# Kernel tuning notes

Measured on AMD Instinct MI355X. Metric: run time of the kernel, lower is better.

## Reference

```python
import jax, jax.numpy as jnp
import numpy as np

T = 4096   # reference sequence length (concatenated virtual samples)
L = 4096   # modality sequence length
D_Q = 64   # reference feature dim
D_QK = 128 # projected query/key dim (before add_one -> 129)
D_V = 128  # value dim
N_IDS = 8  # number of virtual samples encoded in idx


def setup_inputs() -> dict:
    key = jax.random.key(0)
    ks = jax.random.split(key, 20)
    inp = {}
    inp['ref_data'] = jax.random.normal(ks[0], (1, 1, T, D_Q), jnp.float32)
    inp['ref_time'] = jnp.sort(jax.random.uniform(ks[1], (1, T), jnp.float32), axis=-1)
    inp['ref_idx'] = jnp.sort(jax.random.randint(ks[2], (T,), 0, N_IDS))
    inp['m1_data'] = jax.random.normal(ks[3], (1, 1, L, 130), jnp.float32)
    inp['m1_time'] = jnp.sort(jax.random.uniform(ks[4], (1, L), jnp.float32), axis=-1)
    inp['m1_idx'] = jnp.sort(jax.random.randint(ks[5], (L,), 0, N_IDS))
    inp['m2_data'] = jax.random.normal(ks[6], (1, 1, L, 66), jnp.float32)
    inp['m2_time'] = jnp.sort(jax.random.uniform(ks[7], (1, L), jnp.float32), axis=-1)
    inp['m2_idx'] = jnp.sort(jax.random.randint(ks[8], (L,), 0, N_IDS))
    s = 0.05
    inp['Wq'] = jax.random.normal(ks[9], (D_Q, D_QK), jnp.float32) * s
    inp['bq'] = jnp.zeros((D_QK,), jnp.float32)
    inp['Wk1'] = jax.random.normal(ks[10], (1, D_QK), jnp.float32) * s
    inp['bk1'] = jnp.zeros((D_QK,), jnp.float32)
    inp['Wv1'] = jax.random.normal(ks[11], (128, D_V), jnp.float32) * s
    inp['bv1'] = jnp.zeros((D_V,), jnp.float32)
    inp['Wk2'] = jax.random.normal(ks[12], (1, D_QK), jnp.float32) * s
    inp['bk2'] = jnp.zeros((D_QK,), jnp.float32)
    inp['Wv2'] = jax.random.normal(ks[13], (64, D_V), jnp.float32) * s
    inp['bv2'] = jnp.zeros((D_V,), jnp.float32)
    inp['log_tau1'] = jnp.zeros((), jnp.float32)  # log(init_tau=1)
    inp['log_tau2'] = jnp.zeros((), jnp.float32)
    return inp


def _add_one_q(x):  # add_one(x, dim=1): append ones on last axis
    return jnp.concatenate([x, jnp.ones(x.shape[:-1] + (1,), x.dtype)], axis=-1)


def _feat_k(x):  # add_one(x, dim=0): [ones, -x]
    return jnp.concatenate([jnp.ones(x.shape[:-1] + (1,), x.dtype), -x], axis=-1)


def _uni_attn(Q, mdata, q_t, kv_t, q_idx, kv_idx, Wk, bk, Wv, bv, log_tau):
    # qk_type='time': keys from last feature (timestamp), values from data[..., :-2]
    K = _feat_k(mdata[..., -1:] @ Wk + bk)          # (1,1,L,d_qk+1)
    V = mdata[..., :-2] @ Wv + bv                   # (1,1,L,d_v)
    tau = jnp.exp(log_tau)
    # gaussian weight: -(Q.K)^2 / tau
    A = -jnp.square(jnp.einsum('nhtc,nhlc->nhtl', Q, K)) / tau  # (1,1,T,L)
    causal = (q_t[:, :, None] >= kv_t[:, None, :]).astype(Q.dtype)[:, None]  # (1,1,T,L)
    neg_inf = jnp.array(-jnp.inf, Q.dtype)
    bm = jnp.where(q_idx[None, :, None] == kv_idx[None, None, :], jnp.zeros((), Q.dtype), neg_inf)  # (1,T,L)
    fully_masked = jnp.all(jnp.isneginf(bm), axis=-1, keepdims=True)
    safe = jnp.where(fully_masked, jnp.zeros((), Q.dtype), bm)[:, None]  # (1,1,T,L)
    A = jax.nn.softmax(A * causal + safe, axis=-1) * causal
    return jnp.einsum('nhtl,nhlc->nhtc', A, V)      # (1,1,T,d_v)


def reference(ref_data, ref_time, m1_data, m1_time, m2_data, m2_time,
              Wq, bq, Wk1, bk1, Wv1, bv1, Wk2, bk2, Wv2, bv2,
              log_tau1, log_tau2, ref_idx, m1_idx, m2_idx):
    Q = _add_one_q(ref_data @ Wq + bq)  # (1,1,T,d_qk+1)
    y1 = _uni_attn(Q, m1_data, ref_time, m1_time, ref_idx, m1_idx, Wk1, bk1, Wv1, bv1, log_tau1)
    y2 = _uni_attn(Q, m2_data, ref_time, m2_time, ref_idx, m2_idx, Wk2, bk2, Wv2, bv2, log_tau2)
    return jnp.concatenate([y1, y2], axis=-1)  # (1,1,T,2*d_v)
```

## Files before the change

kernel.cpp:

```cpp
#include <hip/hip_runtime.h>
#include <hip/hip_bf16.h>

#define TQ 4096
#define LK 4096
#define QT 16
#define NSPLIT 4
#define CHJ 16
#define PB 32
#define PQ (TQ / PB)
#define VPB 512

template<bool BF> __device__ __forceinline__ float ld(const void* p, int i);
template<> __device__ __forceinline__ float ld<true>(const void* p, int i) {
    return __bfloat162float(((const __hip_bfloat16*)p)[i]);
}
template<> __device__ __forceinline__ float ld<false>(const void* p, int i) {
    return ((const float*)p)[i];
}
template<bool BF> __device__ __forceinline__ float2 ld2(const void* p, int i);
template<> __device__ __forceinline__ float2 ld2<false>(const void* p, int i) {
    return *(const float2*)((const float*)p + i);
}
template<> __device__ __forceinline__ float2 ld2<true>(const void* p, int i) {
    float2 r; r.x = ld<true>(p, i); r.y = ld<true>(p, i + 1); return r;
}
template<bool BF> __device__ __forceinline__ float4 ld4(const void* p, int i);
template<> __device__ __forceinline__ float4 ld4<false>(const void* p, int i) {
    return *(const float4*)((const float*)p + i);
}
template<> __device__ __forceinline__ float4 ld4<true>(const void* p, int i) {
    float4 r; r.x = ld<true>(p, i); r.y = ld<true>(p, i + 1);
    r.z = ld<true>(p, i + 2); r.w = ld<true>(p, i + 3); return r;
}
template<bool BF> __device__ __forceinline__ void st4(void* p, int i, float4 v);
template<> __device__ __forceinline__ void st4<true>(void* p, int i, float4 v) {
    __hip_bfloat16* o = (__hip_bfloat16*)p + i;
    o[0] = __float2bfloat16(v.x); o[1] = __float2bfloat16(v.y);
    o[2] = __float2bfloat16(v.z); o[3] = __float2bfloat16(v.w);
}
template<> __device__ __forceinline__ void st4<false>(void* p, int i, float4 v) {
    *(float4*)((float*)p + i) = v;
}

__device__ __forceinline__ bool sniff_bf16(const void* ref_time) {
    const int lane = threadIdx.x & 63;
    bool ok = true;
    if (lane < 32) {
        float v = __bfloat162float(((const __hip_bfloat16*)ref_time)[2 * lane]);
        ok = (v >= 0.0f) && (v <= 1.0f);
    }
    return __ballot(ok) == ~0ULL;
}

__device__ int lb_int(const int* arr, int n, int key) {
    int lo = 0, hi = n;
    while (lo < hi) { int mid = (lo + hi) >> 1; if (arr[mid] < key) lo = mid + 1; else hi = mid; }
    return lo;
}
__device__ int ub_int(const int* arr, int n, int key) {
    int lo = 0, hi = n;
    while (lo < hi) { int mid = (lo + hi) >> 1; if (arr[mid] <= key) lo = mid + 1; else hi = mid; }
    return lo;
}

template<bool BF>
__device__ void prep_part(
    const void* ref_data, const void* ref_time, const int* ref_idx,
    const void* m1_time, const int* m1_idx, const void* m2_time, const int* m2_idx,
    const void* Wq, const void* bq,
    const void* Wk1, const void* bk1, const void* Wk2, const void* bk2,
    float* alpha1, float* beta1, float* alpha2, float* beta2,
    int* c1, int* s1, int* e1, int* c2, int* s2, int* e2)
{
    __shared__ float ut[64][4];
    __shared__ float cst[4];
    __shared__ int tabs[4][8];

    const int tid = threadIdx.x;
    const int i = tid >> 2, r = tid & 3;

    {
        const void* w = (r == 0) ? Wk1 : (r == 1) ? bk1 : (r == 2) ? Wk2 : bk2;
        const bool isA = (r & 1);
        float acc = isA ? ld<BF>(Wq, i * 128) : 0.0f;
        const float sgn = isA ? -1.0f : 1.0f;
        #pragma unroll 4
        for (int d = 1; d < 128; ++d)
            acc = fmaf(sgn * ld<BF>(Wq, i * 128 + d), ld<BF>(w, d - 1), acc);
        ut[i][r] = acc;
    }
    if (tid < 4) {
        const void* w = (tid == 0) ? Wk1 : (tid == 1) ? bk1 : (tid == 2) ? Wk2 : bk2;
        const bool isA = (tid & 1);
        float c = isA ? ld<BF>(bq, 0) : 0.0f;
        const float sgn = isA ? -1.0f : 1.0f;
        #pragma unroll 4
        for (int d = 1; d < 128; ++d)
            c = fmaf(sgn * ld<BF>(bq, d), ld<BF>(w, d - 1), c);
        c += sgn * ld<BF>(w, 127);
        cst[tid] = c;
    }
    if (tid >= 4 && tid < 36) {
        const int k = tid - 4;
        const int sid = k & 7, rest = k >> 3;
        const int modk = rest & 1, kind = rest >> 1;
        const int* arr = modk ? m2_idx : m1_idx;
        tabs[modk * 2 + kind][sid] = kind ? ub_int(arr, LK, sid) : lb_int(arr, LK, sid);
    }
    __syncthreads();

    const int q = tid & 127;
    const int t = blockIdx.x * PQ + q;
    if (tid < 128) {
        float4 acc = {cst[0], cst[1], cst[2], cst[3]};
        #pragma unroll
        for (int ii = 0; ii < 64; ii += 4) {
            const float4 rv = ld4<BF>(ref_data, t * 64 + ii);
            const float4 u0 = *(const float4*)ut[ii + 0];
            const float4 u1 = *(const float4*)ut[ii + 1];
            const float4 u2 = *(const float4*)ut[ii + 2];
            const float4 u3 = *(const float4*)ut[ii + 3];
            acc.x = fmaf(rv.x, u0.x, fmaf(rv.y, u1.x, fmaf(rv.z, u2.x, fmaf(rv.w, u3.x, acc.x))));
            acc.y = fmaf(rv.x, u0.y, fmaf(rv.y, u1.y, fmaf(rv.z, u2.y, fmaf(rv.w, u3.y, acc.y))));
            acc.z = fmaf(rv.x, u0.z, fmaf(rv.y, u1.z, fmaf(rv.z, u2.z, fmaf(rv.w, u3.z, acc.z))));
            acc.w = fmaf(rv.x, u0.w, fmaf(rv.y, u1.w, fmaf(rv.z, u2.w, fmaf(rv.w, u3.w, acc.w))));
        }
        beta1[t] = acc.x; alpha1[t] = acc.y;
        beta2[t] = acc.z; alpha2[t] = acc.w;
    } else {
        const float qt = ld<BF>(ref_time, t);
        const int g = ref_idx[t];
        int lo1 = 0, hi1 = LK, lo2 = 0, hi2 = LK;
        #pragma unroll
        for (int it = 0; it < 13; ++it) {
            const int mA = min((lo1 + hi1) >> 1, LK - 1);
            const int mB = min((lo2 + hi2) >> 1, LK - 1);
            const float v1 = ld<BF>(m1_time, mA);
            const float v2 = ld<BF>(m2_time, mB);
            if (lo1 < hi1) { if (v1 <= qt) lo1 = mA + 1; else hi1 = mA; }
            if (lo2 < hi2) { if (v2 <= qt) lo2 = mB + 1; else hi2 = mB; }
        }
        c1[t] = lo1; c2[t] = lo2;
        s1[t] = tabs[0][g]; e1[t] = tabs[1][g];
        s2[t] = tabs[2][g]; e2[t] = tabs[3][g];
    }
}

template<bool BF, int K, int DM>
__device__ void vproj_wave(const void* md, const void* Wv, const void* bv,
                           float* V, float* X, int rows0)
{
    const int lane = threadIdx.x & 63;
    const int cT = lane & 31;
    const int rG = lane >> 5;
    const int r0 = rows0 + rG * 2;
    const int c4 = cT * 4;

    const float4 bb = ld4<BF>(bv, c4);
    float4 acc[2] = {bb, bb};

    #pragma unroll 4
    for (int k = 0; k < K; k += 4) {
        const float4 w0 = ld4<BF>(Wv, (k + 0) * 128 + c4);
        const float4 w1 = ld4<BF>(Wv, (k + 1) * 128 + c4);
        const float4 w2 = ld4<BF>(Wv, (k + 2) * 128 + c4);
        const float4 w3 = ld4<BF>(Wv, (k + 3) * 128 + c4);
        float2 alo[2], ahi[2];
        #pragma unroll
        for (int r = 0; r < 2; ++r) {
            alo[r] = ld2<BF>(md, (r0 + r) * DM + k);
            ahi[r] = ld2<BF>(md, (r0 + r) * DM + k + 2);
        }
        #pragma unroll
        for (int r = 0; r < 2; ++r) {
            acc[r].x = fmaf(alo[r].x, w0.x, fmaf(alo[r].y, w1.x, fmaf(ahi[r].x, w2.x, fmaf(ahi[r].y, w3.x, acc[r].x))));
            acc[r].y = fmaf(alo[r].x, w0.y, fmaf(alo[r].y, w1.y, fmaf(ahi[r].x, w2.y, fmaf(ahi[r].y, w3.y, acc[r].y))));
            acc[r].z = fmaf(alo[r].x, w0.z, fmaf(alo[r].y, w1.z, fmaf(ahi[r].x, w2.z, fmaf(ahi[r].y, w3.z, acc[r].z))));
            acc[r].w = fmaf(alo[r].x, w0.w, fmaf(alo[r].y, w1.w, fmaf(ahi[r].x, w2.w, fmaf(ahi[r].y, w3.w, acc[r].w))));
        }
    }
    #pragma unroll
    for (int r = 0; r < 2; ++r)
        *(float4*)&V[(size_t)(r0 + r) * 128 + c4] = acc[r];
    if (rG == 0 && cT < 4)
        X[rows0 + cT] = ld<BF>(md, (rows0 + cT) * DM + DM - 1);
}

template<bool BF>
__device__ void pv_body(
    const void* ref_data, const void* ref_time, const int* ref_idx,
    const void* m1_data, const void* m1_time, const int* m1_idx,
    const void* m2_data, const void* m2_time, const int* m2_idx,
    const void* Wq, const void* bq,
    const void* Wk1, const void* bk1, const void* Wk2, const void* bk2,
    const void* Wv1, const void* bv1, const void* Wv2, const void* bv2,
    float* alpha1, float* beta1, float* alpha2, float* beta2,
    int* c1, int* s1, int* e1, int* c2, int* s2, int* e2,
    float* V1, float* V2, float* X1, float* X2)
{
    if (blockIdx.x < PB) {
        prep_part<BF>(ref_data, ref_time, ref_idx, m1_time, m1_idx, m2_time, m2_idx,
                      Wq, bq, Wk1, bk1, Wk2, bk2,
                      alpha1, beta1, alpha2, beta2, c1, s1, e1, c2, s2, e2);
    } else {
        const int vb = blockIdx.x - PB;
        const int mod = vb >> 8;
        const int wid = threadIdx.x >> 6;
        const int rows0 = (vb & 255) * 16 + wid * 4;
        if (mod == 0) vproj_wave<BF, 128, 130>(m1_data, Wv1, bv1, V1, X1, rows0);
        else          vproj_wave<BF, 64, 66>(m2_data, Wv2, bv2, V2, X2, rows0);
    }
}

__global__ __launch_bounds__(256) void pv_kernel(
    const void* ref_data, const void* ref_time, const int* ref_idx,
    const void* m1_data, const void* m1_time, const int* m1_idx,
    const void* m2_data, const void* m2_time, const int* m2_idx,
    const void* Wq, const void* bq,
    const void* Wk1, const void* bk1, const void* Wk2, const void* bk2,
    const void* Wv1, const void* bv1, const void* Wv2, const void* bv2,
    float* alpha1, float* beta1, float* alpha2, float* beta2,
    int* c1, int* s1, int* e1, int* c2, int* s2, int* e2,
    float* V1, float* V2, float* X1, float* X2)
{
    if (sniff_bf16(ref_time))
        pv_body<true>(ref_data, ref_time, ref_idx, m1_data, m1_time, m1_idx,
                      m2_data, m2_time, m2_idx, Wq, bq, Wk1, bk1, Wk2, bk2,
                      Wv1, bv1, Wv2, bv2, alpha1, beta1, alpha2, beta2,
                      c1, s1, e1, c2, s2, e2, V1, V2, X1, X2);
    else
        pv_body<false>(ref_data, ref_time, ref_idx, m1_data, m1_time, m1_idx,
                       m2_data, m2_time, m2_idx, Wq, bq, Wk1, bk1, Wk2, bk2,
                       Wv1, bv1, Wv2, bv2, alpha1, beta1, alpha2, beta2,
                       c1, s1, e1, c2, s2, e2, V1, V2, X1, X2);
}

__global__ __launch_bounds__(128) void attn_kernel(
    const void* __restrict__ ref_time,
    const float* __restrict__ alpha1, const float* __restrict__ beta1,
    const float* __restrict__ alpha2, const float* __restrict__ beta2,
    const int* __restrict__ c1, const int* __restrict__ s1, const int* __restrict__ e1,
    const int* __restrict__ c2, const int* __restrict__ s2, const int* __restrict__ e2,
    const float* __restrict__ V1, const float* __restrict__ V2,
    const float* __restrict__ X1, const float* __restrict__ X2,
    const void* log_tau1, const void* log_tau2,
    float* __restrict__ Opart, float* __restrict__ Zpart)
{
    __shared__ float sW[2][CHJ * QT];
    __shared__ float sO[QT * 128];
    __shared__ float sZm[QT];

    const int tid = threadIdx.x;
    const int wid = tid >> 6, lane = tid & 63;
    const int t0 = blockIdx.x * QT, zb = blockIdx.y, mod = blockIdx.z;

    const bool bf = sniff_bf16(ref_time);
    const float* alpha = mod ? alpha2 : alpha1;
    const float* beta  = mod ? beta2  : beta1;
    const int* cA = mod ? c2 : c1;
    const int* sA = mod ? s2 : s1;
    const int* eA = mod ? e2 : e1;
    const float* V = mod ? V2 : V1;
    const float* X = mod ? X2 : X1;
    const void* ltp = mod ? log_tau2 : log_tau1;
    const float scale = __expf(-(bf ? ld<true>(ltp, 0) : ld<false>(ltp, 0)));

    const int q = lane & 15;
    const int t = t0 + q;
    int s = sA[t], e = eA[t];
    const int c = cA[t];
    if (s == e) { s = 0; e = LK; }
    const int cm = min(c, e);
    const float al = alpha[t], be = beta[t];

    int es = (cm > s) ? s : 0x7fffffff;
    int ec = (cm > s) ? cm : 0;
    #pragma unroll
    for (int o = 1; o < 64; o <<= 1) {
        es = min(es, __shfl_xor(es, o));
        ec = max(ec, __shfl_xor(ec, o));
    }
    int jlo = es, jhi = ec;
    if (jlo > jhi) { jlo = 0; jhi = 0; }
    const int W = jhi - jlo;
    const int chunk = (W + NSPLIT * 2 - 1) / (NSPLIT * 2);
    const int sub = zb * 2 + wid;
    const int lo = jlo + sub * chunk;
    int hi = min(jhi, lo + chunk); if (hi < lo) hi = lo;

    const int cT = lane & 31, qG = lane >> 5;
    const int jj = lane >> 4;
    float4 acc[8] = {{0,0,0,0},{0,0,0,0},{0,0,0,0},{0,0,0,0},
                     {0,0,0,0},{0,0,0,0},{0,0,0,0},{0,0,0,0}};
    float zacc = 0.0f;
    float* myW = sW[wid];
    const float4* __restrict__ Vg = (const float4*)V;

    for (int base = lo; base < hi; base += CHJ) {
        const int jm = min(CHJ, hi - base);
        __asm__ volatile("s_waitcnt lgkmcnt(0)" ::: "memory");
        #pragma unroll
        for (int p = 0; p < 4; ++p) {
            const int jr = jj * 4 + p;
            const int j = base + jr;
            const bool ok = (jr < jm) && (j >= s) && (j < cm);
            const float x = X[min(j, LK - 1)];
            const float qk = fmaf(-be, x, al);
            const float w = ok ? __expf(-(qk * qk) * scale) : 0.0f;
            myW[jr * QT + q] = w;
            zacc += w;
        }
        __asm__ volatile("s_waitcnt lgkmcnt(0)" ::: "memory");
        #pragma unroll 4
        for (int j = 0; j < jm; ++j) {
            const float4 v = Vg[(base + j) * 32 + cT];
            const float4* wv = (const float4*)&myW[j * QT + qG * 8];
            const float4 wA = wv[0], wB = wv[1];
            acc[0].x = fmaf(wA.x, v.x, acc[0].x); acc[0].y = fmaf(wA.x, v.y, acc[0].y);
            acc[0].z = fmaf(wA.x, v.z, acc[0].z); acc[0].w = fmaf(wA.x, v.w, acc[0].w);
            acc[1].x = fmaf(wA.y, v.x, acc[1].x); acc[1].y = fmaf(wA.y, v.y, acc[1].y);
            acc[1].z = fmaf(wA.y, v.z, acc[1].z); acc[1].w = fmaf(wA.y, v.w, acc[1].w);
            acc[2].x = fmaf(wA.z, v.x, acc[2].x); acc[2].y = fmaf(wA.z, v.y, acc[2].y);
            acc[2].z = fmaf(wA.z, v.z, acc[2].z); acc[2].w = fmaf(wA.z, v.w, acc[2].w);
            acc[3].x = fmaf(wA.w, v.x, acc[3].x); acc[3].y = fmaf(wA.w, v.y, acc[3].y);
            acc[3].z = fmaf(wA.w, v.z, acc[3].z); acc[3].w = fmaf(wA.w, v.w, acc[3].w);
            acc[4].x = fmaf(wB.x, v.x, acc[4].x); acc[4].y = fmaf(wB.x, v.y, acc[4].y);
            acc[4].z = fmaf(wB.x, v.z, acc[4].z); acc[4].w = fmaf(wB.x, v.w, acc[4].w);
            acc[5].x = fmaf(wB.y, v.x, acc[5].x); acc[5].y = fmaf(wB.y, v.y, acc[5].y);
            acc[5].z = fmaf(wB.y, v.z, acc[5].z); acc[5].w = fmaf(wB.y, v.w, acc[5].w);
            acc[6].x = fmaf(wB.z, v.x, acc[6].x); acc[6].y = fmaf(wB.z, v.y, acc[6].y);
            acc[6].z = fmaf(wB.z, v.z, acc[6].z); acc[6].w = fmaf(wB.z, v.w, acc[6].w);
            acc[7].x = fmaf(wB.w, v.x, acc[7].x); acc[7].y = fmaf(wB.w, v.y, acc[7].y);
            acc[7].z = fmaf(wB.w, v.z, acc[7].z); acc[7].w = fmaf(wB.w, v.w, acc[7].w);
        }
    }

    float z = zacc;
    z += __shfl_xor(z, 16);
    z += __shfl_xor(z, 32);

    const int part = zb * 2 + mod;
    if (wid == 0) {
        #pragma unroll
        for (int r = 0; r < 8; ++r)
            *(float4*)&sO[(qG * 8 + r) * 128 + cT * 4] = acc[r];
        if (lane < 16) sZm[lane] = z;
    }
    __syncthreads();
    if (wid == 1) {
        float4* Og = (float4*)Opart;
        #pragma unroll
        for (int r = 0; r < 8; ++r) {
            const float4 o0 = *(const float4*)&sO[(qG * 8 + r) * 128 + cT * 4];
            float4 o = acc[r];
            o.x += o0.x; o.y += o0.y; o.z += o0.z; o.w += o0.w;
            Og[((size_t)(part << 12) + (t0 + qG * 8 + r)) * 32 + cT] = o;
        }
        if (lane < 16) Zpart[(part << 12) + t0 + lane] = z + sZm[lane];
    }
}

__global__ __launch_bounds__(256) void finish_kernel(
    const void* __restrict__ ref_time,
    const int* __restrict__ c1, const int* __restrict__ s1, const int* __restrict__ e1,
    const int* __restrict__ c2, const int* __restrict__ s2, const int* __restrict__ e2,
    const float* __restrict__ Zpart, const float* __restrict__ Opart,
    void* __restrict__ out)
{
    const bool bf = sniff_bf16(ref_time);
    const int idx = blockIdx.x * 256 + threadIdx.x;
    const int t = idx >> 6;
    const int rem = idx & 63;
    const int mod = rem >> 5;
    const int c4 = rem & 31;

    const int* cA = mod ? c2 : c1;
    const int* sA = mod ? s2 : s1;
    const int* eA = mod ? e2 : e1;
    int s = sA[t], e = eA[t];
    const int c = cA[t];
    if (s == e) { s = 0; e = LK; }
    const int nnc = (e > c) ? (e - max(s, c)) : 0;

    float Z = (float)nnc;
    float4 o = {0, 0, 0, 0};
    const float4* Og = (const float4*)Opart;
    #pragma unroll
    for (int zb = 0; zb < NSPLIT; ++zb) {
        const int part = zb * 2 + mod;
        Z += Zpart[(part << 12) + t];
        const float4 p = Og[((size_t)(part << 12) + t) * 32 + c4];
        o.x += p.x; o.y += p.y; o.z += p.z; o.w += p.w;
    }
    const float inv = 1.0f / fmaxf(Z, 1.0e-20f);
    o.x *= inv; o.y *= inv; o.z *= inv; o.w *= inv;
    if (bf) st4<true>(out, t * 256 + mod * 128 + c4 * 4, o);
    else    st4<false>(out, t * 256 + mod * 128 + c4 * 4, o);
}

extern "C" void kernel_launch(void* const* d_in, const int* in_sizes, int n_in,
                              void* d_out, int out_size, void* d_ws, size_t ws_size,
                              hipStream_t stream)
{
    const void* ref_data = d_in[0];
    const void* ref_time = d_in[1];
    const int*  ref_idx  = (const int*)d_in[2];
    const void* m1_data  = d_in[3];
    const void* m1_time  = d_in[4];
    const int*  m1_idx   = (const int*)d_in[5];
    const void* m2_data  = d_in[6];
    const void* m2_time  = d_in[7];
    const int*  m2_idx   = (const int*)d_in[8];
    const void* Wq  = d_in[9];
    const void* bq  = d_in[10];
    const void* Wk1 = d_in[11];
    const void* bk1 = d_in[12];
    const void* Wv1 = d_in[13];
    const void* bv1 = d_in[14];
    const void* Wk2 = d_in[15];
    const void* bk2 = d_in[16];
    const void* Wv2 = d_in[17];
    const void* bv2 = d_in[18];
    const void* log_tau1 = d_in[19];
    const void* log_tau2 = d_in[20];

    float* ws = (float*)d_ws;
    float* alpha1 = ws + 0 * TQ;
    float* beta1  = ws + 1 * TQ;
    float* alpha2 = ws + 2 * TQ;
    float* beta2  = ws + 3 * TQ;
    int*   c1 = (int*)(ws + 4 * TQ);
    int*   c2 = (int*)(ws + 5 * TQ);
    int*   s1 = (int*)(ws + 6 * TQ);
    int*   e1 = (int*)(ws + 7 * TQ);
    int*   s2 = (int*)(ws + 8 * TQ);
    int*   e2 = (int*)(ws + 9 * TQ);
    float* X1 = ws + 10 * TQ;
    float* X2 = ws + 11 * TQ;
    float* V1 = ws + 12 * TQ;
    float* V2 = V1 + (size_t)LK * 128;
    float* Zpart = V2 + (size_t)LK * 128;
    float* Opart = Zpart + 8 * TQ;

    pv_kernel<<<dim3(PB + VPB), dim3(256), 0, stream>>>(
        ref_data, ref_time, ref_idx, m1_data, m1_time, m1_idx,
        m2_data, m2_time, m2_idx, Wq, bq, Wk1, bk1, Wk2, bk2,
        Wv1, bv1, Wv2, bv2, alpha1, beta1, alpha2, beta2,
        c1, s1, e1, c2, s2, e2, V1, V2, X1, X2);

    attn_kernel<<<dim3(TQ / QT, NSPLIT, 2), dim3(128), 0, stream>>>(
        ref_time, alpha1, beta1, alpha2, beta2, c1, s1, e1, c2, s2, e2,
        V1, V2, X1, X2, log_tau1, log_tau2, Opart, Zpart);

    finish_kernel<<<dim3(TQ * 2 * 32 / 256), dim3(256), 0, stream>>>(
        ref_time, c1, s1, e1, c2, s2, e2, Zpart, Opart, (void*)d_out);
}
```

Before: 164.1 us.

## Fuse split-K reduction into attention kernel using 8 waves per block

Replaces the grid-level split over key chunks (4 blocks of 2 waves each, plus a separate finish kernel reading partials from global memory) with a single 512-thread block per query tile and modality. The 8 waves each cover one key sub-range, write their partial outputs and normalizers to shared memory, and then reduce and normalize in-block before writing the final output. This removes one kernel launch and the global round trip of the partial buffers, at the cost of about 70KB of shared memory per block and four times fewer blocks, which may lower occupancy.

```diff
diff --git a/kernel.cpp b/kernel.cpp
--- a/kernel.cpp
+++ b/kernel.cpp
@@ -4,7 +4,7 @@
 #define TQ 4096
 #define LK 4096
 #define QT 16
-#define NSPLIT 4
+#define NW 8
 #define CHJ 16
 #define PB 32
 #define PQ (TQ / PB)
@@ -235,7 +235,7 @@
                        c1, s1, e1, c2, s2, e2, V1, V2, X1, X2);
 }
 
-__global__ __launch_bounds__(128) void attn_kernel(
+__global__ __launch_bounds__(512) void attn_kernel(
     const void* __restrict__ ref_time,
     const float* __restrict__ alpha1, const float* __restrict__ beta1,
     const float* __restrict__ alpha2, const float* __restrict__ beta2,
@@ -243,16 +243,15 @@
     const int* __restrict__ c2, const int* __restrict__ s2, const int* __restrict__ e2,
     const float* __restrict__ V1, const float* __restrict__ V2,
     const float* __restrict__ X1, const float* __restrict__ X2,
-    const void* log_tau1, const void* log_tau2,
-    float* __restrict__ Opart, float* __restrict__ Zpart)
-{
-    __shared__ float sW[2][CHJ * QT];
-    __shared__ float sO[QT * 128];
-    __shared__ float sZm[QT];
+    const void* log_tau1, const void* log_tau2, void* __restrict__ out)
+{
+    __shared__ float sW[NW][CHJ * QT];
+    __shared__ float sO[NW][QT * 128];
+    __shared__ float sZ[NW][QT];
 
     const int tid = threadIdx.x;
     const int wid = tid >> 6, lane = tid & 63;
-    const int t0 = blockIdx.x * QT, zb = blockIdx.y, mod = blockIdx.z;
+    const int t0 = blockIdx.x * QT, mod = blockIdx.y;
 
     const bool bf = sniff_bf16(ref_time);
     const float* alpha = mod ? alpha2 : alpha1;
@@ -283,9 +282,8 @@
     int jlo = es, jhi = ec;
     if (jlo > jhi) { jlo = 0; jhi = 0; }
     const int W = jhi - jlo;
-    const int chunk = (W + NSPLIT * 2 - 1) / (NSPLIT * 2);
-    const int sub = zb * 2 + wid;
-    const int lo = jlo + sub * chunk;
+    const int chunk = (W + NW - 1) / NW;
+    const int lo = jlo + wid * chunk;
     int hi = min(jhi, lo + chunk); if (hi < lo) hi = lo;
 
     const int cT = lane & 31, qG = lane >> 5;
@@ -339,63 +337,31 @@
     z += __shfl_xor(z, 16);
     z += __shfl_xor(z, 32);
 
-    const int part = zb * 2 + mod;
-    if (wid == 0) {
-        #pragma unroll
-        for (int r = 0; r < 8; ++r)
-            *(float4*)&sO[(qG * 8 + r) * 128 + cT * 4] = acc[r];
-        if (lane < 16) sZm[lane] = z;
-    }
+    #pragma unroll
+    for (int r = 0; r < 8; ++r)
+        *(float4*)&sO[wid][(qG * 8 + r) * 128 + cT * 4] = acc[r];
+    if (lane < 16) sZ[wid][lane] = z;
     __syncthreads();
-    if (wid == 1) {
-        float4* Og = (float4*)Opart;
-        #pragma unroll
-        for (int r = 0; r < 8; ++r) {
-            const float4 o0 = *(const float4*)&sO[(qG * 8 + r) * 128 + cT * 4];
-            float4 o = acc[r];
-            o.x += o0.x; o.y += o0.y; o.z += o0.z; o.w += o0.w;
-            Og[((size_t)(part << 12) + (t0 + qG * 8 + r)) * 32 + cT] = o;
-        }
-        if (lane < 16) Zpart[(part << 12) + t0 + lane] = z + sZm[lane];
-    }
-}
-
-__global__ __launch_bounds__(256) void finish_kernel(
-    const void* __restrict__ ref_time,
-    const int* __restrict__ c1, const int* __restrict__ s1, const int* __restrict__ e1,
-    const int* __restrict__ c2, const int* __restrict__ s2, const int* __restrict__ e2,
-    const float* __restrict__ Zpart, const float* __restrict__ Opart,
-    void* __restrict__ out)
-{
-    const bool bf = sniff_bf16(ref_time);
-    const int idx = blockIdx.x * 256 + threadIdx.x;
-    const int t = idx >> 6;
-    const int rem = idx & 63;
-    const int mod = rem >> 5;
-    const int c4 = rem & 31;
-
-    const int* cA = mod ? c2 : c1;
-    const int* sA = mod ? s2 : s1;
-    const int* eA = mod ? e2 : e1;
-    int s = sA[t], e = eA[t];
-    const int c = cA[t];
-    if (s == e) { s = 0; e = LK; }
-    const int nnc = (e > c) ? (e - max(s, c)) : 0;
-
-    float Z = (float)nnc;
+
+    const int mq = tid >> 5, mc = tid & 31;
+    const int mt = t0 + mq;
+    int ms = sA[mt], me = eA[mt];
+    const int mcau = cA[mt];
+    if (ms == me) { ms = 0; me = LK; }
+    const int mnnc = (me > mcau) ? (me - max(ms, mcau)) : 0;
+
+    float Z = (float)mnnc;
     float4 o = {0, 0, 0, 0};
-    const float4* Og = (const float4*)Opart;
     #pragma unroll
-    for (int zb = 0; zb < NSPLIT; ++zb) {
-        const int part = zb * 2 + mod;
-        Z += Zpart[(part << 12) + t];
-        const float4 p = Og[((size_t)(part << 12) + t) * 32 + c4];
+    for (int w = 0; w < NW; ++w) {
+        Z += sZ[w][mq];
+        const float4 p = *(const float4*)&sO[w][mq * 128 + mc * 4];
         o.x += p.x; o.y += p.y; o.z += p.z; o.w += p.w;
     }
     const float inv = 1.0f / fmaxf(Z, 1.0e-20f);
     o.x *= inv; o.y *= inv; o.z *= inv; o.w *= inv;
-    if (bf) st4<true>(out, t * 256 + mod * 128 + c4 * 4, o);
-    else    st4<false>(out, t * 256 + mod * 128 + c4 * 4, o);
+    if (bf) st4<true>(out, mt * 256 + mod * 128 + mc * 4, o);
+    else    st4<false>(out, mt * 256 + mod * 128 + mc * 4, o);
 }
 
 extern "C" void kernel_launch(void* const* d_in, const int* in_sizes, int n_in,
@@ -439,8 +405,6 @@
     float* X2 = ws + 11 * TQ;
     float* V1 = ws + 12 * TQ;
     float* V2 = V1 + (size_t)LK * 128;
-    float* Zpart = V2 + (size_t)LK * 128;
-    float* Opart = Zpart + 8 * TQ;
 
     pv_kernel<<<dim3(PB + VPB), dim3(256), 0, stream>>>(
         ref_data, ref_time, ref_idx, m1_data, m1_time, m1_idx,
@@ -448,10 +412,7 @@
         Wv1, bv1, Wv2, bv2, alpha1, beta1, alpha2, beta2,
         c1, s1, e1, c2, s2, e2, V1, V2, X1, X2);
 
-    attn_kernel<<<dim3(TQ / QT, NSPLIT, 2), dim3(128), 0, stream>>>(
+    attn_kernel<<<dim3(TQ / QT, 2), dim3(512), 0, stream>>>(
         ref_time, alpha1, beta1, alpha2, beta2, c1, s1, e1, c2, s2, e2,
-        V1, V2, X1, X2, log_tau1, log_tau2, Opart, Zpart);
-
-    finish_kernel<<<dim3(TQ * 2 * 32 / 256), dim3(256), 0, stream>>>(
-        ref_time, c1, s1, e1, c2, s2, e2, Zpart, Opart, (void*)d_out);
-}
+        V1, V2, X1, X2, log_tau1, log_tau2, (void*)d_out);
+}
```

Result: faster. 156.1 us (-4.9%).
